# Kernel tuning notes

Measured on AMD Instinct MI355X. Metric: run time of the kernel, lower is better.

## Reference

```python
import jax, jax.numpy as jnp
import numpy as np

NUM_ITEMS = 50000
NUM_USERS = 16384   # static number of user segments (total_user universe)
H0 = 512            # encoder_hidden_size[0]
LAT = 256           # bottleneck (encoder_hidden_size[-1] / decoder_hidden_size[0])
N = 262144          # observed interactions
NT = 262144         # target interactions


def setup_inputs() -> dict:
    key = jax.random.key(0)
    ks = jax.random.split(key, 14)

    def glorot(k, shape):
        fan_in, fan_out = shape[1], shape[0]
        lim = np.sqrt(6.0 / (fan_in + fan_out)).astype(np.float32)
        return jax.random.uniform(k, shape, jnp.float32, -lim, lim)

    return {
        "user": jax.random.randint(ks[0], (N,), 0, NUM_USERS, jnp.int32),
        "item": jax.random.randint(ks[1], (N,), 0, NUM_ITEMS, jnp.int32),
        "rating": jax.random.normal(ks[2], (N,), jnp.float32),
        "target_user": jax.random.randint(ks[3], (NT,), 0, NUM_USERS, jnp.int32),
        "target_item": jax.random.randint(ks[4], (NT,), 0, NUM_ITEMS, jnp.int32),
        "target_rating": jax.random.normal(ks[5], (NT,), jnp.float32),
        # encoder_linear: Linear(num_items, H0)
        "W_enc": glorot(ks[6], (H0, NUM_ITEMS)),
        "b_enc": jnp.zeros((H0,), jnp.float32),
        # Encoder: Linear(H0, LAT) + Tanh
        "W1": glorot(ks[7], (LAT, H0)),
        "b1": jnp.zeros((LAT,), jnp.float32),
        # Decoder: Linear(LAT, H0) + Tanh
        "W2": glorot(ks[8], (H0, LAT)),
        "b2": jnp.zeros((H0,), jnp.float32),
        # decoder_linear: Linear(H0, num_items)
        "W_dec": glorot(ks[9], (NUM_ITEMS, H0)),
        "b_dec": jnp.zeros((NUM_ITEMS,), jnp.float32),
    }


def reference(user, item, rating, target_user, target_item, target_rating,
              W_enc, b_enc, W1, b1, W2, b2, W_dec, b_dec):
    # --- encoder: gather item weight rows, scale by rating, segment-sum per user ---
    # rows: [N, H0] gather from W_enc.T ([NUM_ITEMS, H0])
    rows = W_enc.T[item] * rating[:, None]
    # per-user aggregation over the full user universe (equivalent to the
    # torch unique/sort/index_add path: users with no interactions get 0 -> tanh(bias))
    agg = jax.ops.segment_sum(rows, user, num_segments=NUM_USERS)  # [U, H0]
    x = jnp.tanh(agg + b_enc)
    # --- small dense tanh MLP encoder/decoder ---
    encoded = jnp.tanh(x @ W1.T + b1)          # [U, LAT]
    decoded = jnp.tanh(encoded @ W2.T + b2)    # [U, H0] (dropout = identity, eval mode)
    # --- decoder: gather user codes & item decoder rows, rowwise dot ---
    g = decoded[target_user]                   # [NT, H0]
    w = W_dec[target_item]                     # [NT, H0]
    pred = jnp.sum(g * w, axis=-1) + b_dec[target_item]  # [NT]
    loss = jnp.mean((pred - target_rating) ** 2)
    return pred, loss
```

## Files before the change

### kernel.cpp

```cpp
#include <hip/hip_runtime.h>
#include <hip/hip_bf16.h>
#include <math.h>

#define NUM_ITEMS 50000
#define NUM_USERS 16384
#define H0 512
#define LAT 256
#define FP8_SCALE 64.0f
#define FP8_INV (1.0f / 64.0f)

typedef __attribute__((ext_vector_type(8))) short short8;
typedef __attribute__((ext_vector_type(4))) float floatx4;
typedef __attribute__((ext_vector_type(2))) float vf2;

__device__ __forceinline__ unsigned short f2bf(float f) {
    union { float f; unsigned i; } u; u.f = f;
    unsigned r = u.i + 0x7fff + ((u.i >> 16) & 1);
    return (unsigned short)(r >> 16);
}
__device__ __forceinline__ float bfhi(unsigned v) {
    union { unsigned i; float f; } u; u.i = v & 0xffff0000u; return u.f;
}
__device__ __forceinline__ float bflo(unsigned v) {
    union { unsigned i; float f; } u; u.i = v << 16; return u.f;
}
__device__ __forceinline__ uint4 pack8(const float* v) {
    uint4 p;
    p.x = (unsigned)f2bf(v[0]) | ((unsigned)f2bf(v[1]) << 16);
    p.y = (unsigned)f2bf(v[2]) | ((unsigned)f2bf(v[3]) << 16);
    p.z = (unsigned)f2bf(v[4]) | ((unsigned)f2bf(v[5]) << 16);
    p.w = (unsigned)f2bf(v[6]) | ((unsigned)f2bf(v[7]) << 16);
    return p;
}
__device__ __forceinline__ unsigned pkfp8_4(float a, float b, float c, float d) {
    int v = __builtin_amdgcn_cvt_pk_fp8_f32(a, b, 0, false);
    v = __builtin_amdgcn_cvt_pk_fp8_f32(c, d, v, true);
    return (unsigned)v;
}
__device__ __forceinline__ void fp8x4_to_f32(unsigned v, float* o) {
    vf2 lo = __builtin_amdgcn_cvt_pk_f32_fp8((int)v, false);
    vf2 hi = __builtin_amdgcn_cvt_pk_f32_fp8((int)v, true);
    o[0] = lo.x; o[1] = lo.y; o[2] = hi.x; o[3] = hi.y;
}

__global__ __launch_bounds__(256) void count_kernel(const int* __restrict__ user, int* __restrict__ cntU,
                                                    const int* __restrict__ t_user, int* __restrict__ cntTU,
                                                    int n, int nt) {
    int i = (blockIdx.x * blockDim.x + threadIdx.x) * 4;
    if (i + 3 < n) {
        int4 u = *(const int4*)(user + i);
        atomicAdd(&cntU[u.x], 1); atomicAdd(&cntU[u.y], 1);
        atomicAdd(&cntU[u.z], 1); atomicAdd(&cntU[u.w], 1);
    } else {
        for (int k = i; k < n; ++k) atomicAdd(&cntU[user[k]], 1);
    }
    if (i + 3 < nt) {
        int4 t = *(const int4*)(t_user + i);
        atomicAdd(&cntTU[t.x], 1); atomicAdd(&cntTU[t.y], 1);
        atomicAdd(&cntTU[t.z], 1); atomicAdd(&cntTU[t.w], 1);
    } else {
        for (int k = i; k < nt; ++k) atomicAdd(&cntTU[t_user[k]], 1);
    }
}

__device__ void scan_block(const int* __restrict__ cnt, int* __restrict__ offs,
                           int* __restrict__ cursor, int per) {
    __shared__ int ssum[1024];
    int t = threadIdx.x;
    int base = t * per;
    int s = 0;
    for (int j = 0; j < per; j += 4) {
        int4 v = *(const int4*)(cnt + base + j);
        s += v.x + v.y + v.z + v.w;
    }
    ssum[t] = s;
    __syncthreads();
    for (int off = 1; off < 1024; off <<= 1) {
        int v = (t >= off) ? ssum[t - off] : 0;
        __syncthreads();
        ssum[t] += v;
        __syncthreads();
    }
    int run = (t == 0) ? 0 : ssum[t - 1];
    for (int j = 0; j < per; j += 4) {
        int4 v = *(const int4*)(cnt + base + j);
        int4 o;
        o.x = run; run += v.x;
        o.y = run; run += v.y;
        o.z = run; run += v.z;
        o.w = run; run += v.w;
        *(int4*)(offs + base + j) = o;
        *(int4*)(cursor + base + j) = o;
    }
}

__global__ void scan_kernel(const int* __restrict__ cntU, int* __restrict__ offsU, int* __restrict__ curU,
                            const int* __restrict__ cntTU, int* __restrict__ offsTU, int* __restrict__ curTU) {
    if (blockIdx.x == 0) scan_block(cntU, offsU, curU, NUM_USERS / 1024);
    else scan_block(cntTU, offsTU, curTU, NUM_USERS / 1024);
}

__global__ __launch_bounds__(256) void mega_kernel(
        const int* __restrict__ user, const int* __restrict__ item,
        const float* __restrict__ rating, int* __restrict__ curU, int2* __restrict__ s_pack,
        const int* __restrict__ t_user, const int* __restrict__ t_item,
        const float* __restrict__ t_rating, int* __restrict__ curTU, int4* __restrict__ st_pack,
        const float* __restrict__ W_enc, unsigned char* __restrict__ wtb8,
        const float* __restrict__ W_dec, unsigned char* __restrict__ wdb8,
        const float* __restrict__ W1, unsigned short* __restrict__ w1b,
        const float* __restrict__ W2, unsigned short* __restrict__ w2b,
        int n, int nt, int SB, int TB, int DB) {
    __shared__ float tileh[64 * 64];
    int bid = blockIdx.x;
    int tid = threadIdx.x;
    if (bid < SB) {
        int i = bid * 256 + tid;
        if (i < n) {
            int u = user[i];
            int pos = atomicAdd(&curU[u], 1);
            s_pack[pos] = make_int2(item[i], __float_as_int(rating[i]));
        }
        if (i < nt) {
            int tu = t_user[i];
            int pos = atomicAdd(&curTU[tu], 1);
            st_pack[pos] = make_int4(t_item[i], __float_as_int(t_rating[i]), i, 0);
        }
    } else if (bid < SB + TB) {
        const int TBX = (NUM_ITEMS + 63) / 64;
        int b = bid - SB;
        int x0 = (b % TBX) * 64;
        int y0 = (b / TBX) * 64;
        int g = tid >> 4;
        int m = tid & 15;
        int it4 = x0 + m * 4;
#pragma unroll
        for (int p = 0; p < 4; ++p) {
            int hloc = p * 16 + g;
            if (it4 < NUM_ITEMS) {
                float4 v = *(const float4*)(W_enc + (size_t)(y0 + hloc) * NUM_ITEMS + it4);
                *(float4*)(tileh + hloc * 64 + m * 4) = v;
            }
        }
        __syncthreads();
        int i = tid >> 2;
        int l = tid & 3;
        int it = x0 + i;
        if (it < NUM_ITEMS) {
            const float* src = tileh + (l * 16) * 64 + i;
            uint4 o;
            o.x = pkfp8_4(src[0] * FP8_SCALE, src[64] * FP8_SCALE, src[128] * FP8_SCALE, src[192] * FP8_SCALE);
            o.y = pkfp8_4(src[256] * FP8_SCALE, src[320] * FP8_SCALE, src[384] * FP8_SCALE, src[448] * FP8_SCALE);
            o.z = pkfp8_4(src[512] * FP8_SCALE, src[576] * FP8_SCALE, src[640] * FP8_SCALE, src[704] * FP8_SCALE);
            o.w = pkfp8_4(src[768] * FP8_SCALE, src[832] * FP8_SCALE, src[896] * FP8_SCALE, src[960] * FP8_SCALE);
            *(uint4*)(wtb8 + (size_t)it * H0 + y0 + l * 16) = o;
        }
    } else if (bid < SB + TB + DB) {
        size_t idx = (size_t)(bid - SB - TB) * 4096 + tid * 16;
        float4 v0 = *(const float4*)(W_dec + idx);
        float4 v1 = *(const float4*)(W_dec + idx + 4);
        float4 v2 = *(const float4*)(W_dec + idx + 8);
        float4 v3 = *(const float4*)(W_dec + idx + 12);
        uint4 o;
        o.x = pkfp8_4(v0.x * FP8_SCALE, v0.y * FP8_SCALE, v0.z * FP8_SCALE, v0.w * FP8_SCALE);
        o.y = pkfp8_4(v1.x * FP8_SCALE, v1.y * FP8_SCALE, v1.z * FP8_SCALE, v1.w * FP8_SCALE);
        o.z = pkfp8_4(v2.x * FP8_SCALE, v2.y * FP8_SCALE, v2.z * FP8_SCALE, v2.w * FP8_SCALE);
        o.w = pkfp8_4(v3.x * FP8_SCALE, v3.y * FP8_SCALE, v3.z * FP8_SCALE, v3.w * FP8_SCALE);
        *(uint4*)(wdb8 + idx) = o;
    } else {
        int b2i = bid - SB - TB - DB;
        const float* src = (b2i < 64) ? W1 : W2;
        unsigned short* dst = (b2i < 64) ? w1b : w2b;
        int idx = (b2i & 63) * 2048 + tid * 8;
        float v[8];
        *(float4*)&v[0] = *(const float4*)(src + idx);
        *(float4*)&v[4] = *(const float4*)(src + idx + 4);
        *(uint4*)(dst + idx) = pack8(v);
    }
}

__global__ __launch_bounds__(256) void agg_kernel(const unsigned char* __restrict__ wtb8,
                                                  const int* __restrict__ offs,
                                                  const int* __restrict__ ends,
                                                  const int2* __restrict__ s_pack,
                                                  const float* __restrict__ b_enc,
                                                  unsigned short* __restrict__ xb) {
    __shared__ float red[3 * 512];
    int u = blockIdx.x;
    int tid = threadIdx.x;
    int g = tid >> 6, lane = tid & 63;
    float acc[8] = {};
    int j0 = offs[u], j1 = ends[u];
    int j = j0 + g;
    int2 nxt = (j < j1) ? s_pack[j] : make_int2(0, 0);
    while (j < j1) {
        int2 cur = nxt;
        int jn = j + 4;
        if (jn < j1) nxt = s_pack[jn];
        float r = __int_as_float(cur.y);
        uint2 v = ((const uint2*)(wtb8 + (size_t)cur.x * H0))[lane];
        float wf[8];
        fp8x4_to_f32(v.x, wf);
        fp8x4_to_f32(v.y, wf + 4);
#pragma unroll
        for (int e = 0; e < 8; ++e) acc[e] += wf[e] * r;
        j = jn;
    }
    if (g) {
        float4* rp = (float4*)red + (size_t)(g - 1) * 128 + lane * 2;
        rp[0] = make_float4(acc[0], acc[1], acc[2], acc[3]);
        rp[1] = make_float4(acc[4], acc[5], acc[6], acc[7]);
    }
    __syncthreads();
    if (g == 0) {
#pragma unroll
        for (int h = 0; h < 3; ++h) {
            const float* rp = red + h * 512 + lane * 8;
#pragma unroll
            for (int e = 0; e < 8; ++e) acc[e] += rp[e];
        }
        float4 b0 = ((const float4*)b_enc)[lane * 2];
        float4 b1 = ((const float4*)b_enc)[lane * 2 + 1];
        float o[8];
        o[0] = tanhf(acc[0] * FP8_INV + b0.x); o[1] = tanhf(acc[1] * FP8_INV + b0.y);
        o[2] = tanhf(acc[2] * FP8_INV + b0.z); o[3] = tanhf(acc[3] * FP8_INV + b0.w);
        o[4] = tanhf(acc[4] * FP8_INV + b1.x); o[5] = tanhf(acc[5] * FP8_INV + b1.y);
        o[6] = tanhf(acc[6] * FP8_INV + b1.z); o[7] = tanhf(acc[7] * FP8_INV + b1.w);
        ((uint4*)(xb + (size_t)u * H0))[lane] = pack8(o);
    }
}

template<int BN>
__global__ __launch_bounds__(256) void gemm_mfma(const unsigned short* __restrict__ A,
                                                 const unsigned short* __restrict__ B,
                                                 const float* __restrict__ bias,
                                                 unsigned short* __restrict__ C,
                                                 int Nn, int K) {
    constexpr int WN = BN / 32;
    constexpr int NCH = 8 + BN / 16;
    constexpr int PER = NCH / 4;
    __shared__ unsigned short Ash[128 * 32];
    __shared__ unsigned short Bsh[BN * 32];
    int tid = threadIdx.x;
    int wid = tid >> 6, lane = tid & 63;
    int wave_m = wid & 1, wave_n = wid >> 1;
    int quad = lane >> 4, l16 = lane & 15;
    int m0 = blockIdx.x * 128, n0 = blockIdx.y * BN;
    floatx4 acc[4][WN] = {};
    int srow = lane >> 2;
    int scol = (lane & 3) * 8;
    for (int k0 = 0; k0 < K; k0 += 32) {
#pragma unroll
        for (int i = 0; i < PER; ++i) {
            int c = wid * PER + i;
            if (c < 8) {
                const unsigned short* ga = A + (size_t)(m0 + c * 16 + srow) * K + k0 + scol;
                __builtin_amdgcn_global_load_lds(
                    (const __attribute__((address_space(1))) void*)ga,
                    (__attribute__((address_space(3))) void*)((__attribute__((address_space(3))) char*)Ash + c * 1024),
                    16, 0, 0);
            } else {
                const unsigned short* gb = B + (size_t)(n0 + (c - 8) * 16 + srow) * K + k0 + scol;
                __builtin_amdgcn_global_load_lds(
                    (const __attribute__((address_space(1))) void*)gb,
                    (__attribute__((address_space(3))) void*)((__attribute__((address_space(3))) char*)Bsh + (c - 8) * 1024),
                    16, 0, 0);
            }
        }
        __syncthreads();
        short8 af[4], bfr[WN];
#pragma unroll
        for (int i = 0; i < 4; ++i) {
            int ml = wave_m * 64 + i * 16 + l16;
            af[i] = ((const short8*)Ash)[ml * 4 + quad];
        }
#pragma unroll
        for (int j = 0; j < WN; ++j) {
            int nl = wave_n * (BN / 2) + j * 16 + l16;
            bfr[j] = ((const short8*)Bsh)[nl * 4 + quad];
        }
#pragma unroll
        for (int i = 0; i < 4; ++i)
#pragma unroll
            for (int j = 0; j < WN; ++j)
                acc[i][j] = __builtin_amdgcn_mfma_f32_16x16x32_bf16(af[i], bfr[j], acc[i][j], 0, 0, 0);
        __syncthreads();
    }
#pragma unroll
    for (int j = 0; j < WN; ++j) {
        int col = n0 + wave_n * (BN / 2) + j * 16 + l16;
        float bv = bias[col];
#pragma unroll
        for (int i = 0; i < 4; ++i) {
            int rowb = m0 + wave_m * 64 + i * 16 + quad * 4;
#pragma unroll
            for (int r = 0; r < 4; ++r)
                C[(size_t)(rowb + r) * Nn + col] = f2bf(tanhf(acc[i][j][r] + bv));
        }
    }
}

__global__ __launch_bounds__(256) void predict_kernel(const unsigned short* __restrict__ dec_b,
                                                      const unsigned char* __restrict__ wdb8,
                                                      const float* __restrict__ b_dec,
                                                      const int* __restrict__ offs,
                                                      const int* __restrict__ ends,
                                                      const int4* __restrict__ st,
                                                      float* __restrict__ pred,
                                                      float* __restrict__ partials) {
    __shared__ float wsum[4];
    int u = blockIdx.x;
    int wid = threadIdx.x >> 6, lane = threadIdx.x & 63;
    int j0 = offs[u], j1 = ends[u];
    float sq = 0.f;
    if (j0 < j1) {
        uint4 gv = ((const uint4*)(dec_b + (size_t)u * H0))[lane];
        float g[8];
        g[0] = bflo(gv.x); g[1] = bfhi(gv.x);
        g[2] = bflo(gv.y); g[3] = bfhi(gv.y);
        g[4] = bflo(gv.z); g[5] = bfhi(gv.z);
        g[6] = bflo(gv.w); g[7] = bfhi(gv.w);
        int j = j0 + wid;
        int4 tv = (j < j1) ? st[j] : make_int4(0, 0, 0, 0);
        uint2 wv = make_uint2(0, 0);
        if (j < j1) wv = ((const uint2*)(wdb8 + (size_t)tv.x * H0))[lane];
        while (j < j1) {
            int jn = j + 4;
            int4 tvn = make_int4(0, 0, 0, 0);
            uint2 wvn = make_uint2(0, 0);
            if (jn < j1) {
                tvn = st[jn];
                wvn = ((const uint2*)(wdb8 + (size_t)tvn.x * H0))[lane];
            }
            float wf[8];
            fp8x4_to_f32(wv.x, wf);
            fp8x4_to_f32(wv.y, wf + 4);
            float s = g[0] * wf[0] + g[1] * wf[1] + g[2] * wf[2] + g[3] * wf[3]
                    + g[4] * wf[4] + g[5] * wf[5] + g[6] * wf[6] + g[7] * wf[7];
#pragma unroll
            for (int off = 32; off; off >>= 1) s += __shfl_xor(s, off, 64);
            if (lane == 0) {
                float p = s * FP8_INV + b_dec[tv.x];
                pred[tv.z] = p;
                float d = p - __int_as_float(tv.y);
                sq += d * d;
            }
            j = jn; tv = tvn; wv = wvn;
        }
    }
    if (lane == 0) wsum[wid] = sq;
    __syncthreads();
    if (threadIdx.x == 0)
        partials[u] = wsum[0] + wsum[1] + wsum[2] + wsum[3];
}

__global__ void loss_reduce(const float* __restrict__ partials, float* __restrict__ out_loss,
                            int nPart, float invNT) {
    __shared__ float s[256];
    int t = threadIdx.x;
    float a = 0.f;
    const float4* p4 = (const float4*)partials;
    int n4 = nPart >> 2;
    for (int i = t; i < n4; i += 256) {
        float4 v = p4[i];
        a += v.x + v.y + v.z + v.w;
    }
    for (int i = (n4 << 2) + t; i < nPart; i += 256) a += partials[i];
    s[t] = a;
    __syncthreads();
    for (int off = 128; off; off >>= 1) {
        if (t < off) s[t] += s[t + off];
        __syncthreads();
    }
    if (t == 0) out_loss[0] = s[0] * invNT;
}

extern "C" void kernel_launch(void* const* d_in, const int* in_sizes, int n_in,
                              void* d_out, int out_size, void* d_ws, size_t ws_size,
                              hipStream_t stream) {
    const int* user = (const int*)d_in[0];
    const int* item = (const int*)d_in[1];
    const float* rating = (const float*)d_in[2];
    const int* t_user = (const int*)d_in[3];
    const int* t_item = (const int*)d_in[4];
    const float* t_rating = (const float*)d_in[5];
    const float* W_enc = (const float*)d_in[6];
    const float* b_enc = (const float*)d_in[7];
    const float* W1 = (const float*)d_in[8];
    const float* b1 = (const float*)d_in[9];
    const float* W2 = (const float*)d_in[10];
    const float* b2 = (const float*)d_in[11];
    const float* W_dec = (const float*)d_in[12];
    const float* b_dec = (const float*)d_in[13];
    const int N = in_sizes[0];
    const int NT = in_sizes[3];

    char* ws = (char*)d_ws;
    size_t off = 0;
    auto alloc = [&](size_t bytes) {
        void* p = ws + off;
        off = (off + bytes + 255) & ~(size_t)255;
        return p;
    };
    unsigned char* wtb8 = (unsigned char*)alloc((size_t)NUM_ITEMS * H0);
    unsigned char* wdb8 = (unsigned char*)alloc((size_t)NUM_ITEMS * H0);
    unsigned short* xb = (unsigned short*)alloc((size_t)NUM_USERS * H0 * 2);
    unsigned short* enc_b = (unsigned short*)alloc((size_t)NUM_USERS * LAT * 2);
    unsigned short* dec_b = (unsigned short*)alloc((size_t)NUM_USERS * H0 * 2);
    unsigned short* w1b = (unsigned short*)alloc((size_t)LAT * H0 * 2);
    unsigned short* w2b = (unsigned short*)alloc((size_t)H0 * LAT * 2);
    int* cntU = (int*)alloc((size_t)NUM_USERS * 2 * 4);
    int* cntTU = cntU + NUM_USERS;
    int* offsU = (int*)alloc((size_t)NUM_USERS * 4);
    int* curU = (int*)alloc((size_t)NUM_USERS * 4);
    int* offsTU = (int*)alloc((size_t)NUM_USERS * 4);
    int* curTU = (int*)alloc((size_t)NUM_USERS * 4);
    int2* s_pack = (int2*)alloc((size_t)N * 8);
    int4* st_pack = (int4*)alloc((size_t)NT * 16);
    float* partials = (float*)alloc((size_t)NUM_USERS * 4);

    float* pred = (float*)d_out;
    float* loss = pred + NT;

    const int maxNNT = N > NT ? N : NT;
    const int SB = (maxNNT + 255) / 256;
    const int TBX = (NUM_ITEMS + 63) / 64;
    const int TB = TBX * (H0 / 64);
    const int DB = (NUM_ITEMS * H0) / 4096;
    const int WB = 128;

    hipMemsetAsync(cntU, 0, (size_t)NUM_USERS * 2 * 4, stream);
    count_kernel<<<(maxNNT + 1023) / 1024, 256, 0, stream>>>(user, cntU, t_user, cntTU, N, NT);
    scan_kernel<<<2, 1024, 0, stream>>>(cntU, offsU, curU, cntTU, offsTU, curTU);
    mega_kernel<<<SB + TB + DB + WB, 256, 0, stream>>>(
        user, item, rating, curU, s_pack,
        t_user, t_item, t_rating, curTU, st_pack,
        W_enc, wtb8, W_dec, wdb8, W1, w1b, W2, w2b,
        N, NT, SB, TB, DB);
    agg_kernel<<<NUM_USERS, 256, 0, stream>>>(wtb8, offsU, curU, s_pack, b_enc, xb);
    gemm_mfma<64><<<dim3(NUM_USERS / 128, LAT / 64), 256, 0, stream>>>(xb, w1b, b1, enc_b, LAT, H0);
    gemm_mfma<64><<<dim3(NUM_USERS / 128, H0 / 64), 256, 0, stream>>>(enc_b, w2b, b2, dec_b, H0, LAT);
    predict_kernel<<<NUM_USERS, 256, 0, stream>>>(dec_b, wdb8, b_dec, offsTU, curTU, st_pack, pred, partials);
    loss_reduce<<<1, 256, 0, stream>>>(partials, loss, NUM_USERS, 1.0f / NT);
}
```

Baseline: 422.3 us.

## Split mega kernel, swizzle transpose LDS, wave-shuffle scan, double agg loads

Splits the combined scatter/transpose/cast mega kernel into three separate launches. The W_enc transpose tile gets a rotated LDS layout to cut bank conflicts, and the scan switches from a shared-memory Hillis-Steele loop to wave shuffles. The aggregation loop now issues two gathered row loads per iteration for more memory-level parallelism. The split adds launch overhead and removes overlap between the scatter and weight-conversion work.

```diff
diff --git a/kernel.cpp b/kernel.cpp
--- a/kernel.cpp
+++ b/kernel.cpp
@@ -64,98 +64,122 @@
 }
 
 __device__ void scan_block(const int* __restrict__ cnt, int* __restrict__ offs,
-                           int* __restrict__ cursor, int per) {
-    __shared__ int ssum[1024];
+                           int* __restrict__ cursor) {
+    __shared__ int wsum_s[16];
     int t = threadIdx.x;
-    int base = t * per;
-    int s = 0;
-    for (int j = 0; j < per; j += 4) {
-        int4 v = *(const int4*)(cnt + base + j);
-        s += v.x + v.y + v.z + v.w;
-    }
-    ssum[t] = s;
-    __syncthreads();
-    for (int off = 1; off < 1024; off <<= 1) {
-        int v = (t >= off) ? ssum[t - off] : 0;
-        __syncthreads();
-        ssum[t] += v;
-        __syncthreads();
-    }
-    int run = (t == 0) ? 0 : ssum[t - 1];
-    for (int j = 0; j < per; j += 4) {
-        int4 v = *(const int4*)(cnt + base + j);
-        int4 o;
-        o.x = run; run += v.x;
-        o.y = run; run += v.y;
-        o.z = run; run += v.z;
-        o.w = run; run += v.w;
-        *(int4*)(offs + base + j) = o;
-        *(int4*)(cursor + base + j) = o;
-    }
+    int lane = t & 63, wid = t >> 6;
+    int base = t * 16;
+    int4 a = *(const int4*)(cnt + base);
+    int4 b = *(const int4*)(cnt + base + 4);
+    int4 c = *(const int4*)(cnt + base + 8);
+    int4 d = *(const int4*)(cnt + base + 12);
+    int s = a.x + a.y + a.z + a.w + b.x + b.y + b.z + b.w
+          + c.x + c.y + c.z + c.w + d.x + d.y + d.z + d.w;
+    int sc = s;
+#pragma unroll
+    for (int off = 1; off < 64; off <<= 1) {
+        int v = __shfl_up(sc, off, 64);
+        if (lane >= off) sc += v;
+    }
+    if (lane == 63) wsum_s[wid] = sc;
+    __syncthreads();
+    if (t < 16) {
+        int w = wsum_s[t];
+        int wsc = w;
+#pragma unroll
+        for (int off = 1; off < 16; off <<= 1) {
+            int v = __shfl_up(wsc, off, 64);
+            if (t >= off) wsc += v;
+        }
+        wsum_s[t] = wsc - w;
+    }
+    __syncthreads();
+    int run = wsum_s[wid] + (sc - s);
+    int4 o;
+    o.x = run; run += a.x; o.y = run; run += a.y; o.z = run; run += a.z; o.w = run; run += a.w;
+    *(int4*)(offs + base) = o; *(int4*)(cursor + base) = o;
+    o.x = run; run += b.x; o.y = run; run += b.y; o.z = run; run += b.z; o.w = run; run += b.w;
+    *(int4*)(offs + base + 4) = o; *(int4*)(cursor + base + 4) = o;
+    o.x = run; run += c.x; o.y = run; run += c.y; o.z = run; run += c.z; o.w = run; run += c.w;
+    *(int4*)(offs + base + 8) = o; *(int4*)(cursor + base + 8) = o;
+    o.x = run; run += d.x; o.y = run; run += d.y; o.z = run; run += d.z; o.w = run; run += d.w;
+    *(int4*)(offs + base + 12) = o; *(int4*)(cursor + base + 12) = o;
 }
 
 __global__ void scan_kernel(const int* __restrict__ cntU, int* __restrict__ offsU, int* __restrict__ curU,
                             const int* __restrict__ cntTU, int* __restrict__ offsTU, int* __restrict__ curTU) {
-    if (blockIdx.x == 0) scan_block(cntU, offsU, curU, NUM_USERS / 1024);
-    else scan_block(cntTU, offsTU, curTU, NUM_USERS / 1024);
-}
-
-__global__ __launch_bounds__(256) void mega_kernel(
+    if (blockIdx.x == 0) scan_block(cntU, offsU, curU);
+    else scan_block(cntTU, offsTU, curTU);
+}
+
+__global__ __launch_bounds__(256) void scatter_kernel(
         const int* __restrict__ user, const int* __restrict__ item,
         const float* __restrict__ rating, int* __restrict__ curU, int2* __restrict__ s_pack,
         const int* __restrict__ t_user, const int* __restrict__ t_item,
         const float* __restrict__ t_rating, int* __restrict__ curTU, int4* __restrict__ st_pack,
-        const float* __restrict__ W_enc, unsigned char* __restrict__ wtb8,
-        const float* __restrict__ W_dec, unsigned char* __restrict__ wdb8,
-        const float* __restrict__ W1, unsigned short* __restrict__ w1b,
-        const float* __restrict__ W2, unsigned short* __restrict__ w2b,
-        int n, int nt, int SB, int TB, int DB) {
+        int n, int nt) {
+    int i = blockIdx.x * 256 + threadIdx.x;
+    if (i < n) {
+        int u = user[i];
+        int pos = atomicAdd(&curU[u], 1);
+        s_pack[pos] = make_int2(item[i], __float_as_int(rating[i]));
+    }
+    if (i < nt) {
+        int tu = t_user[i];
+        int pos = atomicAdd(&curTU[tu], 1);
+        st_pack[pos] = make_int4(t_item[i], __float_as_int(t_rating[i]), i, 0);
+    }
+}
+
+__global__ __launch_bounds__(256) void transpose_kernel(const float* __restrict__ W_enc,
+                                                        unsigned char* __restrict__ wtb8) {
     __shared__ float tileh[64 * 64];
+    const int TBX = (NUM_ITEMS + 63) / 64;
+    int b = blockIdx.x;
+    int x0 = (b % TBX) * 64;
+    int y0 = (b / TBX) * 64;
+    int tid = threadIdx.x;
+    int g = tid >> 4;
+    int m = tid & 15;
+    int it4 = x0 + m * 4;
+#pragma unroll
+    for (int p = 0; p < 4; ++p) {
+        int hloc = p * 16 + g;
+        if (it4 < NUM_ITEMS) {
+            float4 v = *(const float4*)(W_enc + (size_t)(y0 + hloc) * NUM_ITEMS + it4);
+            int cb = (m * 4 + ((hloc >> 2) << 2)) & 63;
+            *(float4*)(tileh + hloc * 64 + cb) = v;
+        }
+    }
+    __syncthreads();
+    int i = tid >> 2;
+    int l = tid & 3;
+    int it = x0 + i;
+    if (it < NUM_ITEMS) {
+        float f[16];
+#pragma unroll
+        for (int k = 0; k < 16; ++k) {
+            int h = l * 16 + k;
+            f[k] = tileh[h * 64 + ((i + ((h >> 2) << 2)) & 63)];
+        }
+        uint4 o;
+        o.x = pkfp8_4(f[0] * FP8_SCALE, f[1] * FP8_SCALE, f[2] * FP8_SCALE, f[3] * FP8_SCALE);
+        o.y = pkfp8_4(f[4] * FP8_SCALE, f[5] * FP8_SCALE, f[6] * FP8_SCALE, f[7] * FP8_SCALE);
+        o.z = pkfp8_4(f[8] * FP8_SCALE, f[9] * FP8_SCALE, f[10] * FP8_SCALE, f[11] * FP8_SCALE);
+        o.w = pkfp8_4(f[12] * FP8_SCALE, f[13] * FP8_SCALE, f[14] * FP8_SCALE, f[15] * FP8_SCALE);
+        *(uint4*)(wtb8 + (size_t)it * H0 + y0 + l * 16) = o;
+    }
+}
+
+__global__ __launch_bounds__(256) void cast_kernel(const float* __restrict__ W_dec,
+                                                   unsigned char* __restrict__ wdb8,
+                                                   const float* __restrict__ W1, unsigned short* __restrict__ w1b,
+                                                   const float* __restrict__ W2, unsigned short* __restrict__ w2b,
+                                                   int DB) {
     int bid = blockIdx.x;
     int tid = threadIdx.x;
-    if (bid < SB) {
-        int i = bid * 256 + tid;
-        if (i < n) {
-            int u = user[i];
-            int pos = atomicAdd(&curU[u], 1);
-            s_pack[pos] = make_int2(item[i], __float_as_int(rating[i]));
-        }
-        if (i < nt) {
-            int tu = t_user[i];
-            int pos = atomicAdd(&curTU[tu], 1);
-            st_pack[pos] = make_int4(t_item[i], __float_as_int(t_rating[i]), i, 0);
-        }
-    } else if (bid < SB + TB) {
-        const int TBX = (NUM_ITEMS + 63) / 64;
-        int b = bid - SB;
-        int x0 = (b % TBX) * 64;
-        int y0 = (b / TBX) * 64;
-        int g = tid >> 4;
-        int m = tid & 15;
-        int it4 = x0 + m * 4;
-#pragma unroll
-        for (int p = 0; p < 4; ++p) {
-            int hloc = p * 16 + g;
-            if (it4 < NUM_ITEMS) {
-                float4 v = *(const float4*)(W_enc + (size_t)(y0 + hloc) * NUM_ITEMS + it4);
-                *(float4*)(tileh + hloc * 64 + m * 4) = v;
-            }
-        }
-        __syncthreads();
-        int i = tid >> 2;
-        int l = tid & 3;
-        int it = x0 + i;
-        if (it < NUM_ITEMS) {
-            const float* src = tileh + (l * 16) * 64 + i;
-            uint4 o;
-            o.x = pkfp8_4(src[0] * FP8_SCALE, src[64] * FP8_SCALE, src[128] * FP8_SCALE, src[192] * FP8_SCALE);
-            o.y = pkfp8_4(src[256] * FP8_SCALE, src[320] * FP8_SCALE, src[384] * FP8_SCALE, src[448] * FP8_SCALE);
-            o.z = pkfp8_4(src[512] * FP8_SCALE, src[576] * FP8_SCALE, src[640] * FP8_SCALE, src[704] * FP8_SCALE);
-            o.w = pkfp8_4(src[768] * FP8_SCALE, src[832] * FP8_SCALE, src[896] * FP8_SCALE, src[960] * FP8_SCALE);
-            *(uint4*)(wtb8 + (size_t)it * H0 + y0 + l * 16) = o;
-        }
-    } else if (bid < SB + TB + DB) {
-        size_t idx = (size_t)(bid - SB - TB) * 4096 + tid * 16;
+    if (bid < DB) {
+        size_t idx = (size_t)bid * 4096 + tid * 16;
         float4 v0 = *(const float4*)(W_dec + idx);
         float4 v1 = *(const float4*)(W_dec + idx + 4);
         float4 v2 = *(const float4*)(W_dec + idx + 8);
@@ -167,7 +191,7 @@
         o.w = pkfp8_4(v3.x * FP8_SCALE, v3.y * FP8_SCALE, v3.z * FP8_SCALE, v3.w * FP8_SCALE);
         *(uint4*)(wdb8 + idx) = o;
     } else {
-        int b2i = bid - SB - TB - DB;
+        int b2i = bid - DB;
         const float* src = (b2i < 64) ? W1 : W2;
         unsigned short* dst = (b2i < 64) ? w1b : w2b;
         int idx = (b2i & 63) * 2048 + tid * 8;
@@ -191,19 +215,29 @@
     float acc[8] = {};
     int j0 = offs[u], j1 = ends[u];
     int j = j0 + g;
-    int2 nxt = (j < j1) ? s_pack[j] : make_int2(0, 0);
+    int2 c0 = (j < j1) ? s_pack[j] : make_int2(0, 0);
+    int2 c1 = (j + 4 < j1) ? s_pack[j + 4] : make_int2(0, 0);
     while (j < j1) {
-        int2 cur = nxt;
-        int jn = j + 4;
-        if (jn < j1) nxt = s_pack[jn];
-        float r = __int_as_float(cur.y);
-        uint2 v = ((const uint2*)(wtb8 + (size_t)cur.x * H0))[lane];
+        bool has1 = (j + 4) < j1;
+        uint2 v0 = ((const uint2*)(wtb8 + (size_t)c0.x * H0))[lane];
+        uint2 v1 = has1 ? ((const uint2*)(wtb8 + (size_t)c1.x * H0))[lane] : make_uint2(0, 0);
+        int jn = j + 8;
+        int2 n0 = (jn < j1) ? s_pack[jn] : make_int2(0, 0);
+        int2 n1 = (jn + 4 < j1) ? s_pack[jn + 4] : make_int2(0, 0);
+        float r0 = __int_as_float(c0.y);
         float wf[8];
-        fp8x4_to_f32(v.x, wf);
-        fp8x4_to_f32(v.y, wf + 4);
-#pragma unroll
-        for (int e = 0; e < 8; ++e) acc[e] += wf[e] * r;
-        j = jn;
+        fp8x4_to_f32(v0.x, wf);
+        fp8x4_to_f32(v0.y, wf + 4);
+#pragma unroll
+        for (int e = 0; e < 8; ++e) acc[e] += wf[e] * r0;
+        if (has1) {
+            float r1 = __int_as_float(c1.y);
+            fp8x4_to_f32(v1.x, wf);
+            fp8x4_to_f32(v1.y, wf + 4);
+#pragma unroll
+            for (int e = 0; e < 8; ++e) acc[e] += wf[e] * r1;
+        }
+        c0 = n0; c1 = n1; j = jn;
     }
     if (g) {
         float4* rp = (float4*)red + (size_t)(g - 1) * 128 + lane * 2;
@@ -431,11 +465,10 @@
     hipMemsetAsync(cntU, 0, (size_t)NUM_USERS * 2 * 4, stream);
     count_kernel<<<(maxNNT + 1023) / 1024, 256, 0, stream>>>(user, cntU, t_user, cntTU, N, NT);
     scan_kernel<<<2, 1024, 0, stream>>>(cntU, offsU, curU, cntTU, offsTU, curTU);
-    mega_kernel<<<SB + TB + DB + WB, 256, 0, stream>>>(
-        user, item, rating, curU, s_pack,
-        t_user, t_item, t_rating, curTU, st_pack,
-        W_enc, wtb8, W_dec, wdb8, W1, w1b, W2, w2b,
-        N, NT, SB, TB, DB);
+    scatter_kernel<<<SB, 256, 0, stream>>>(user, item, rating, curU, s_pack,
+                                           t_user, t_item, t_rating, curTU, st_pack, N, NT);
+    transpose_kernel<<<TB, 256, 0, stream>>>(W_enc, wtb8);
+    cast_kernel<<<DB + WB, 256, 0, stream>>>(W_dec, wdb8, W1, w1b, W2, w2b, DB);
     agg_kernel<<<NUM_USERS, 256, 0, stream>>>(wtb8, offsU, curU, s_pack, b_enc, xb);
     gemm_mfma<64><<<dim3(NUM_USERS / 128, LAT / 64), 256, 0, stream>>>(xb, w1b, b1, enc_b, LAT, H0);
     gemm_mfma<64><<<dim3(NUM_USERS / 128, H0 / 64), 256, 0, stream>>>(enc_b, w2b, b2, dec_b, H0, LAT);
```

Result: no change. 427.8 us (+1.3%).
